# Kernel optimization log

Hardware: AMD Instinct MI355X
Metric: run time of the kernel (lower is better)

## Reference

```python
import jax, jax.numpy as jnp
import numpy as np

B, C, D, H, W = 4, 256, 16, 16, 16
INTER = C // 8  # 32


def setup_inputs() -> dict:
    key = jax.random.key(0)
    ks = jax.random.split(key, 8)
    return {
        "x": jax.random.normal(ks[0], (B, C, D, H, W), dtype=jnp.float32),
        "Wq": jax.random.normal(ks[1], (INTER, C), dtype=jnp.float32) * 0.05,
        "bq": jax.random.normal(ks[2], (INTER,), dtype=jnp.float32) * 0.05,
        "Wk": jax.random.normal(ks[3], (INTER, C), dtype=jnp.float32) * 0.05,
        "bk": jax.random.normal(ks[4], (INTER,), dtype=jnp.float32) * 0.05,
        "Wv": jax.random.normal(ks[5], (C, C), dtype=jnp.float32) * 0.05,
        "bv": jax.random.normal(ks[6], (C,), dtype=jnp.float32) * 0.05,
        "gamma": jax.random.normal(ks[7], (1,), dtype=jnp.float32),
    }


def reference(x, Wq, bq, Wk, bk, Wv, bv, gamma):
    b, c, d, h, w = x.shape
    n = d * h * w
    xf = x.reshape(b, c, n)  # [B, C, N]
    # 1x1 Conv3d == pointwise channel projection
    q = jnp.einsum("oc,bcn->bon", Wq, xf) + bq[None, :, None]  # [B, inter, N]
    k = jnp.einsum("oc,bcn->bon", Wk, xf) + bk[None, :, None]  # [B, inter, N]
    v = jnp.einsum("oc,bcn->bon", Wv, xf) + bv[None, :, None]  # [B, C, N]
    scale = float(q.shape[1]) ** 0.5
    # attn[b, i, j] = <q[:, i], k[:, j]>
    attn = jax.nn.softmax(jnp.einsum("bci,bcj->bij", q, k) / scale, axis=-1)
    # out[b, c, i] = sum_j v[b, c, j] * attn[b, i, j]
    out = jnp.einsum("bcj,bij->bci", v, attn).reshape(b, c, d, h, w)
    return gamma[0] * out + x
```

## Files before the change

kernel.cpp:

```cpp
#include <hip/hip_runtime.h>

#define B_ 4
#define C_ 256
#define N_ 4096
#define INTER_ 32

typedef __attribute__((ext_vector_type(8))) short short8;
typedef __attribute__((ext_vector_type(4))) float f32x4;
typedef __attribute__((ext_vector_type(16))) float f32x16;
typedef __attribute__((ext_vector_type(4))) unsigned int u32x4;

#define TILEB 18432
#define NSTG  (8 * TILEB)

static __device__ __forceinline__ unsigned short f2bf(float f) {
    unsigned int u = __builtin_bit_cast(unsigned int, f);
    u += 0x7fff + ((u >> 16) & 1);
    return (unsigned short)(u >> 16);
}

static __device__ __forceinline__ unsigned int cvtpk(float lo, float hi) {
    unsigned int r;
    asm("v_cvt_pk_bf16_f32 %0, %1, %2" : "=v"(r) : "v"(lo), "v"(hi));
    return r;
}

static __device__ __forceinline__ void pl32swap(unsigned int& a, unsigned int& b) {
    asm("v_permlane32_swap_b32 %0, %1" : "+v"(a), "+v"(b));
}

static __device__ __forceinline__ void gload16(const void* g, void* l) {
    __builtin_amdgcn_global_load_lds(
        (const __attribute__((address_space(1))) void*)g,
        (__attribute__((address_space(3))) void*)l, 16, 0, 0);
}

__global__ __launch_bounds__(256) void prep_kernel(
    const float* __restrict__ Wq, const float* __restrict__ Wk,
    const float* __restrict__ Wv, unsigned short* __restrict__ wb)
{
    int i = blockIdx.x * 256 + threadIdx.x;
    int row = i >> 8, col = i & 255;
    float v;
    if (row < 32)      v = Wq[row * 256 + col];
    else if (row < 64) v = Wk[(row - 32) * 256 + col];
    else               v = Wv[(row - 64) * 256 + col];
    wb[i] = f2bf(v);
}

__global__ __launch_bounds__(256) void qkv_kernel(
    const float* __restrict__ x, const unsigned short* __restrict__ wb,
    const float* __restrict__ bq, const float* __restrict__ bk,
    const float* __restrict__ bv,
    unsigned short* __restrict__ qb, unsigned short* __restrict__ kfrag,
    unsigned short* __restrict__ vfrag)
{
    const int tid  = threadIdx.x;
    const int wave = tid >> 6;
    const int lane = tid & 63;
    const int l31  = lane & 31;
    const int h2   = lane >> 5;
    const int b    = blockIdx.x >> 6;
    const int n0   = (blockIdx.x & 63) * 64;

    __shared__ unsigned int xsh[64 * 129];

    {
        const float* xb = x + ((size_t)b * C_ + 64 * wave) * N_ + n0 + lane;
        unsigned int* dst = xsh + (size_t)lane * 129 + 32 * wave;
        #pragma unroll 8
        for (int s = 0; s < 32; ++s) {
            float v0 = xb[(size_t)(2 * s) * N_];
            float v1 = xb[(size_t)(2 * s + 1) * N_];
            dst[s] = (unsigned int)f2bf(v0) | ((unsigned int)f2bf(v1) << 16);
        }
    }
    __syncthreads();

    const float rs = 0.17677669529663687f;

    #pragma unroll
    for (int u = 0; u < 5; ++u) {
        const int unit = wave + 4 * u;
        const int ch = unit >> 1;
        const int ns = unit & 1;
        const int ncol = n0 + 32 * ns + l31;
        const int jt = (n0 >> 5) + ns;

        const float* bias = (ch == 0) ? bq : (ch == 1) ? bk : (bv + (ch - 2) * 32);
        f32x16 acc;
        #pragma unroll
        for (int r = 0; r < 16; ++r)
            acc[r] = bias[(r & 3) + 8 * (r >> 2) + 4 * h2];

        const unsigned short* wrow = wb + ((size_t)(ch * 32 + l31)) * 256 + 8 * h2;
        const unsigned int*   xrow = xsh + (size_t)(32 * ns + l31) * 129 + 4 * h2;

        #pragma unroll
        for (int kk = 0; kk < 16; ++kk) {
            short8 wa = *reinterpret_cast<const short8*>(wrow + 16 * kk);
            short8 xf = *reinterpret_cast<const short8*>(xrow + 8 * kk);
            acc = __builtin_amdgcn_mfma_f32_32x32x16_bf16(wa, xf, acc, 0, 0, 0);
        }

        if (ch == 0) {
            unsigned short* dst = qb + ((size_t)b * N_ + ncol) * 32;
            #pragma unroll
            for (int q = 0; q < 4; ++q) {
                unsigned int w0 = (unsigned int)f2bf(acc[4 * q] * rs)
                                | ((unsigned int)f2bf(acc[4 * q + 1] * rs) << 16);
                unsigned int w1 = (unsigned int)f2bf(acc[4 * q + 2] * rs)
                                | ((unsigned int)f2bf(acc[4 * q + 3] * rs) << 16);
                unsigned int* p = reinterpret_cast<unsigned int*>(dst + 4 * h2 + 8 * q);
                p[0] = w0; p[1] = w1;
            }
        } else if (ch == 1) {
            unsigned short* kt = kfrag + ((size_t)b * 128 + jt) * 1024;
            #pragma unroll
            for (int r = 0; r < 16; ++r) {
                const int co = (r & 3) + 8 * (r >> 2) + 4 * h2;
                const int addr = ((co >> 4) << 9) + ((l31 + 32 * ((co >> 3) & 1)) << 3)
                               + (co & 7);
                kt[addr] = f2bf(acc[r]);
            }
        } else {
            const int g = ch - 2;
            unsigned short* vt_ = vfrag + (((size_t)b * 128 + jt) * 8 + g) * 1024;
            #pragma unroll
            for (int r = 0; r < 16; ++r) {
                const int co = (r & 3) + 8 * (r >> 2) + 4 * h2;
                const int addr = ((l31 >> 4) << 9) + ((co + 32 * ((l31 >> 3) & 1)) << 3)
                               + (l31 & 7);
                vt_[addr] = f2bf(acc[r]);
            }
        }
    }
}

__global__ __launch_bounds__(512) void attn_kernel(
    const unsigned short* __restrict__ qb, const unsigned short* __restrict__ kfrag,
    const unsigned short* __restrict__ vfrag,
    const float* __restrict__ x, const float* __restrict__ gamma,
    float* __restrict__ out)
{
    const int tid  = threadIdx.x;
    const int wave = tid >> 6;
    const int lane = tid & 63;
    const int l31  = lane & 31;
    const int h2   = lane >> 5;
    const int jq   = wave >> 1;
    const int qs   = wave & 1;
    const int b    = blockIdx.y;
    const int iq   = blockIdx.x * 64 + 32 * qs;

    __shared__ char lds[NSTG];
    __shared__ float m_sh[8][32];
    __shared__ float l_sh[8][32];

    const unsigned short* vtb = vfrag + (size_t)b * 128 * 8192;
    const unsigned short* ktb = kfrag + (size_t)b * 128 * 1024;

    char* reg0 = lds + (jq * 2) * TILEB;
    char* reg1 = reg0 + TILEB;

    short8 qf0 = *reinterpret_cast<const short8*>(
        qb + ((size_t)b * N_ + iq + l31) * 32 + 8 * h2);
    short8 qf1 = *reinterpret_cast<const short8*>(
        qb + ((size_t)b * N_ + iq + l31) * 32 + 8 * h2 + 16);

    f32x16 acc[8];
    #pragma unroll
    for (int g = 0; g < 8; ++g)
        #pragma unroll
        for (int r = 0; r < 16; ++r) acc[g][r] = 0.f;

    float m_run = 0.f;
    float l_run = 0.f;
    const f32x16 z16 = {};

    {
        const char* vs = (const char*)(vtb + (size_t)(jq * 32) * 8192);
        const char* ks = (const char*)(ktb + (size_t)(jq * 32) * 1024);
        #pragma unroll
        for (int s2 = 0; s2 < 9; ++s2) {
            const int off = qs * 9216 + s2 * 1024;
            const char* g = (off < 16384) ? (vs + off) : (ks + (off - 16384));
            gload16(g + lane * 16, reg0 + off);
        }
    }
    __syncthreads();

    #pragma unroll 1
    for (int t = 0; t < 32; ++t) {
        char* cur = (t & 1) ? reg1 : reg0;
        char* nxt = (t & 1) ? reg0 : reg1;

        if (t < 31) {
            const int jtg = jq * 32 + t + 1;
            const char* vs = (const char*)(vtb + (size_t)jtg * 8192);
            const char* ks = (const char*)(ktb + (size_t)jtg * 1024);
            #pragma unroll
            for (int s2 = 0; s2 < 9; ++s2) {
                const int off = qs * 9216 + s2 * 1024;
                const char* g = (off < 16384) ? (vs + off) : (ks + (off - 16384));
                gload16(g + lane * 16, nxt + off);
            }
        }

        const char* kt_ = cur + 16384;
        short8 ka0 = *reinterpret_cast<const short8*>(kt_ + lane * 16);
        short8 ka1 = *reinterpret_cast<const short8*>(kt_ + 1024 + lane * 16);
        f32x16 s = __builtin_amdgcn_mfma_f32_32x32x16_bf16(ka0, qf0, z16, 0, 0, 0);
        s = __builtin_amdgcn_mfma_f32_32x32x16_bf16(ka1, qf1, s, 0, 0, 0);

        float a0 = fmaxf(s[0], s[8]),  a1 = fmaxf(s[1], s[9]);
        float a2 = fmaxf(s[2], s[10]), a3 = fmaxf(s[3], s[11]);
        float a4 = fmaxf(s[4], s[12]), a5 = fmaxf(s[5], s[13]);
        float a6 = fmaxf(s[6], s[14]), a7 = fmaxf(s[7], s[15]);
        a0 = fmaxf(a0, a4); a1 = fmaxf(a1, a5); a2 = fmaxf(a2, a6); a3 = fmaxf(a3, a7);
        float smax = fmaxf(fmaxf(a0, a1), fmaxf(a2, a3));

        if (__any(smax > m_run + 5.5f)) {
            float sm2 = fmaxf(smax, __shfl_xor(smax, 32));
            float mnew = fmaxf(m_run, sm2);
            float corr = __expf(m_run - mnew);
            m_run = mnew;
            l_run *= corr;
            #pragma unroll
            for (int g = 0; g < 8; ++g)
                #pragma unroll
                for (int r = 0; r < 16; ++r) acc[g][r] *= corr;
        }

        float p[16];
        float lsum = 0.f;
        #pragma unroll
        for (int r = 0; r < 16; ++r) { p[r] = __expf(s[r] - m_run); lsum += p[r]; }
        l_run += lsum;

        unsigned int X0 = cvtpk(p[0],  p[1]),  X1 = cvtpk(p[2],  p[3]);
        unsigned int Y0 = cvtpk(p[4],  p[5]),  Y1 = cvtpk(p[6],  p[7]);
        unsigned int W0 = cvtpk(p[8],  p[9]),  W1 = cvtpk(p[10], p[11]);
        unsigned int V0 = cvtpk(p[12], p[13]), V1 = cvtpk(p[14], p[15]);
        pl32swap(X0, Y0); pl32swap(X1, Y1);
        pl32swap(W0, V0); pl32swap(W1, V1);
        short8 pb0 = __builtin_bit_cast(short8, u32x4{X0, X1, Y0, Y1});
        short8 pb1 = __builtin_bit_cast(short8, u32x4{W0, W1, V0, V1});

        __builtin_amdgcn_s_setprio(1);
        #pragma unroll
        for (int g = 0; g < 8; ++g) {
            short8 va0 = *reinterpret_cast<const short8*>(cur + g * 2048 + lane * 16);
            short8 va1 = *reinterpret_cast<const short8*>(cur + g * 2048 + 1024 + lane * 16);
            acc[g] = __builtin_amdgcn_mfma_f32_32x32x16_bf16(va0, pb0, acc[g], 0, 0, 0);
            acc[g] = __builtin_amdgcn_mfma_f32_32x32x16_bf16(va1, pb1, acc[g], 0, 0, 0);
        }
        __builtin_amdgcn_s_setprio(0);

        __syncthreads();
    }

    float l_tot = l_run + __shfl_xor(l_run, 32);
    if (lane < 32) { m_sh[wave][lane] = m_run; l_sh[wave][lane] = l_tot; }
    __syncthreads();

    float M = -1e30f, L = 0.f;
    #pragma unroll
    for (int w2 = 0; w2 < 4; ++w2) M = fmaxf(M, m_sh[w2 * 2 + qs][l31]);
    #pragma unroll
    for (int w2 = 0; w2 < 4; ++w2)
        L += __expf(m_sh[w2 * 2 + qs][l31] - M) * l_sh[w2 * 2 + qs][l31];
    const float wgt = __expf(m_run - M);
    #pragma unroll
    for (int g = 0; g < 8; ++g)
        #pragma unroll
        for (int r = 0; r < 16; ++r) acc[g][r] *= wgt;

    if (jq >= 2) {
        f32x4* Dr = (f32x4*)(lds + ((jq - 2) * 2 + qs) * 32768);
        #pragma unroll
        for (int g = 0; g < 8; ++g)
            #pragma unroll
            for (int r4 = 0; r4 < 4; ++r4) {
                f32x4 tv;
                #pragma unroll
                for (int e = 0; e < 4; ++e) tv[e] = acc[g][4 * r4 + e];
                Dr[(g * 4 + r4) * 64 + lane] = tv;
            }
    }
    __syncthreads();
    if (jq < 2) {
        const f32x4* Dr = (const f32x4*)(lds + (jq * 2 + qs) * 32768);
        #pragma unroll
        for (int g = 0; g < 8; ++g)
            #pragma unroll
            for (int r4 = 0; r4 < 4; ++r4) {
                f32x4 tv = Dr[(g * 4 + r4) * 64 + lane];
                #pragma unroll
                for (int e = 0; e < 4; ++e) acc[g][4 * r4 + e] += tv[e];
            }
    }
    __syncthreads();
    if (jq == 1) {
        f32x4* Dr = (f32x4*)(lds + (2 + qs) * 32768);
        #pragma unroll
        for (int g = 0; g < 8; ++g)
            #pragma unroll
            for (int r4 = 0; r4 < 4; ++r4) {
                f32x4 tv;
                #pragma unroll
                for (int e = 0; e < 4; ++e) tv[e] = acc[g][4 * r4 + e];
                Dr[(g * 4 + r4) * 64 + lane] = tv;
            }
    }
    __syncthreads();
    if (jq == 0) {
        const f32x4* Dr = (const f32x4*)(lds + (2 + qs) * 32768);
        f32x4* Dw = (f32x4*)(lds + qs * 32768);
        #pragma unroll
        for (int g = 0; g < 8; ++g)
            #pragma unroll
            for (int r4 = 0; r4 < 4; ++r4) {
                f32x4 tv = Dr[(g * 4 + r4) * 64 + lane];
                #pragma unroll
                for (int e = 0; e < 4; ++e) tv[e] += acc[g][4 * r4 + e];
                Dw[(g * 4 + r4) * 64 + lane] = tv;
            }
    }
    __syncthreads();

    const float gma  = gamma[0];
    const float invL = 1.f / L;
    const f32x4* Ds = (const f32x4*)(lds + qs * 32768);
    const int i = iq + l31;
    #pragma unroll
    for (int gi = 0; gi < 2; ++gi) {
        const int g = jq * 2 + gi;
        #pragma unroll
        for (int r4 = 0; r4 < 4; ++r4) {
            f32x4 v = Ds[(g * 4 + r4) * 64 + lane];
            #pragma unroll
            for (int e = 0; e < 4; ++e) {
                const int c = 32 * g + e + 8 * r4 + 4 * h2;
                const size_t off = ((size_t)b * C_ + c) * N_ + i;
                out[off] = gma * v[e] * invL + x[off];
            }
        }
    }
}

extern "C" void kernel_launch(void* const* d_in, const int* in_sizes, int n_in,
                              void* d_out, int out_size, void* d_ws, size_t ws_size,
                              hipStream_t stream) {
    const float* x     = (const float*)d_in[0];
    const float* Wq    = (const float*)d_in[1];
    const float* bq    = (const float*)d_in[2];
    const float* Wk    = (const float*)d_in[3];
    const float* bk    = (const float*)d_in[4];
    const float* Wv    = (const float*)d_in[5];
    const float* bv    = (const float*)d_in[6];
    const float* gamma = (const float*)d_in[7];
    float* out = (float*)d_out;

    unsigned short* ws = (unsigned short*)d_ws;
    unsigned short* qb    = ws;
    unsigned short* kfrag = qb + (size_t)B_ * N_ * INTER_;
    unsigned short* vfrag = kfrag + (size_t)B_ * 128 * 1024;
    unsigned short* wb    = vfrag + (size_t)B_ * 128 * 8192;

    prep_kernel<<<dim3(320), 256, 0, stream>>>(Wq, Wk, Wv, wb);
    qkv_kernel<<<dim3(B_ * (N_ / 64)), 256, 0, stream>>>(
        x, wb, bq, bk, bv, qb, kfrag, vfrag);
    attn_kernel<<<dim3(N_ / 64, B_), 512, 0, stream>>>(
        qb, kfrag, vfrag, x, gamma, out);
}
```

Baseline: 84.60 us.

## Fold log2e into q scale, use exp2, remap blocks per XCD, split loads

Folds log2(e) into the query prescale so softmax can use exp2f directly instead of __expf, and raises the lazy-rescale threshold to match the base-2 exponent. Flattens the attention grid and maps block ids so each batch's blocks land on a pair of XCDs, so the K/V tiles are shared in that XCD's L2. It also reorganises the per-wave staging loads so each wave loads contiguous V chunks and one wave handles the K tile. The risks are a remapping that assumes round-robin dispatch of blocks across 8 XCDs, and slightly different rounding from the base-2 rescaling.

```diff
diff --git a/kernel.cpp b/kernel.cpp
--- a/kernel.cpp
+++ b/kernel.cpp
@@ -77,7 +77,7 @@
     }
     __syncthreads();
 
-    const float rs = 0.17677669529663687f;
+    const float rs = 0.25504183f;
 
     #pragma unroll
     for (int u = 0; u < 5; ++u) {
@@ -150,8 +150,13 @@
     const int h2   = lane >> 5;
     const int jq   = wave >> 1;
     const int qs   = wave & 1;
-    const int b    = blockIdx.y;
-    const int iq   = blockIdx.x * 64 + 32 * qs;
+
+    const int bid  = blockIdx.x;
+    const int xcd  = bid & 7;
+    const int slot = bid >> 3;
+    const int b    = xcd >> 1;
+    const int ib   = slot * 2 + (xcd & 1);
+    const int iq   = ib * 64 + 32 * qs;
 
     __shared__ char lds[NSTG];
     __shared__ float m_sh[8][32];
@@ -179,13 +184,19 @@
     const f32x16 z16 = {};
 
     {
-        const char* vs = (const char*)(vtb + (size_t)(jq * 32) * 8192);
-        const char* ks = (const char*)(ktb + (size_t)(jq * 32) * 1024);
-        #pragma unroll
-        for (int s2 = 0; s2 < 9; ++s2) {
-            const int off = qs * 9216 + s2 * 1024;
-            const char* g = (off < 16384) ? (vs + off) : (ks + (off - 16384));
-            gload16(g + lane * 16, reg0 + off);
+        const int jtg = jq * 32;
+        const char* vs = (const char*)(vtb + (size_t)jtg * 8192);
+        if (qs == 0) {
+            #pragma unroll
+            for (int s2 = 0; s2 < 9; ++s2)
+                gload16(vs + s2 * 1024 + lane * 16, reg0 + s2 * 1024);
+        } else {
+            #pragma unroll
+            for (int s2 = 9; s2 < 16; ++s2)
+                gload16(vs + s2 * 1024 + lane * 16, reg0 + s2 * 1024);
+            const char* ks = (const char*)(ktb + (size_t)jtg * 1024);
+            gload16(ks + lane * 16, reg0 + 16384);
+            gload16(ks + 1024 + lane * 16, reg0 + 17408);
         }
     }
     __syncthreads();
@@ -198,12 +209,17 @@
         if (t < 31) {
             const int jtg = jq * 32 + t + 1;
             const char* vs = (const char*)(vtb + (size_t)jtg * 8192);
-            const char* ks = (const char*)(ktb + (size_t)jtg * 1024);
-            #pragma unroll
-            for (int s2 = 0; s2 < 9; ++s2) {
-                const int off = qs * 9216 + s2 * 1024;
-                const char* g = (off < 16384) ? (vs + off) : (ks + (off - 16384));
-                gload16(g + lane * 16, nxt + off);
+            if (qs == 0) {
+                #pragma unroll
+                for (int s2 = 0; s2 < 9; ++s2)
+                    gload16(vs + s2 * 1024 + lane * 16, nxt + s2 * 1024);
+            } else {
+                #pragma unroll
+                for (int s2 = 9; s2 < 16; ++s2)
+                    gload16(vs + s2 * 1024 + lane * 16, nxt + s2 * 1024);
+                const char* ks = (const char*)(ktb + (size_t)jtg * 1024);
+                gload16(ks + lane * 16, nxt + 16384);
+                gload16(ks + 1024 + lane * 16, nxt + 17408);
             }
         }
 
@@ -220,10 +236,10 @@
         a0 = fmaxf(a0, a4); a1 = fmaxf(a1, a5); a2 = fmaxf(a2, a6); a3 = fmaxf(a3, a7);
         float smax = fmaxf(fmaxf(a0, a1), fmaxf(a2, a3));
 
-        if (__any(smax > m_run + 5.5f)) {
+        if (__any(smax > m_run + 8.0f)) {
             float sm2 = fmaxf(smax, __shfl_xor(smax, 32));
             float mnew = fmaxf(m_run, sm2);
-            float corr = __expf(m_run - mnew);
+            float corr = exp2f(m_run - mnew);
             m_run = mnew;
             l_run *= corr;
             #pragma unroll
@@ -235,7 +251,7 @@
         float p[16];
         float lsum = 0.f;
         #pragma unroll
-        for (int r = 0; r < 16; ++r) { p[r] = __expf(s[r] - m_run); lsum += p[r]; }
+        for (int r = 0; r < 16; ++r) { p[r] = exp2f(s[r] - m_run); lsum += p[r]; }
         l_run += lsum;
 
         unsigned int X0 = cvtpk(p[0],  p[1]),  X1 = cvtpk(p[2],  p[3]);
@@ -269,8 +285,8 @@
     for (int w2 = 0; w2 < 4; ++w2) M = fmaxf(M, m_sh[w2 * 2 + qs][l31]);
     #pragma unroll
     for (int w2 = 0; w2 < 4; ++w2)
-        L += __expf(m_sh[w2 * 2 + qs][l31] - M) * l_sh[w2 * 2 + qs][l31];
-    const float wgt = __expf(m_run - M);
+        L += exp2f(m_sh[w2 * 2 + qs][l31] - M) * l_sh[w2 * 2 + qs][l31];
+    const float wgt = exp2f(m_run - M);
     #pragma unroll
     for (int g = 0; g < 8; ++g)
         #pragma unroll
@@ -371,6 +387,6 @@
     prep_kernel<<<dim3(320), 256, 0, stream>>>(Wq, Wk, Wv, wb);
     qkv_kernel<<<dim3(B_ * (N_ / 64)), 256, 0, stream>>>(
         x, wb, bq, bk, bv, qb, kfrag, vfrag);
-    attn_kernel<<<dim3(N_ / 64, B_), 512, 0, stream>>>(
+    attn_kernel<<<dim3(256), 512, 0, stream>>>(
         qb, kfrag, vfrag, x, gamma, out);
 }
```

Measured after the change: 89.97 us. 1.06x slower.
